# Kernel tuning notes

Hardware: AMD Instinct MI355X
Metric: run time of the kernel (lower is better)

Reference implementation:

```python
import jax, jax.numpy as jnp
import numpy as np


def _conv1x1(x, w, b):
    # x: (B,C,H,W), w: (O,C), b: (O,)
    return jnp.einsum('bchw,oc->bohw', x, w) + b[None, :, None, None]


def setup_inputs() -> dict:
    key = jax.random.key(0)
    ks = jax.random.split(key, 10)
    B, C, H, W = 8, 64, 64, 64
    x = jax.random.normal(ks[0], (B, C, H, W), dtype=jnp.float32)
    s = 0.05
    params = {}
    names = ['wq', 'wQ', 'wK', 'wV']
    for i, n in enumerate(names):
        params[n] = jax.random.normal(ks[1 + 2 * i], (C, C), dtype=jnp.float32) * s
        params['b' + n[1:]] = jax.random.normal(ks[2 + 2 * i], (C,), dtype=jnp.float32) * s
    return dict(x=x, wq=params['wq'], bq=params['bq'], wQ=params['wQ'], bQ=params['bQ'],
                wK=params['wK'], bK=params['bK'], wV=params['wV'], bV=params['bV'],
                gamma=jnp.ones((1,), dtype=jnp.float32))


def reference(x, wq, bq, wQ, bQ, wK, bK, wV, bV, gamma):
    B, C, H, W = x.shape
    # q = query_conv(x).view(B,-1,W,H)  (pure reshape, matches torch .view on contiguous tensor)
    q = _conv1x1(x, wq, bq).reshape(B, C, W, H)
    # 2x2 average pool, stride 2
    qp = q.reshape(B, C, W // 2, 2, H // 2, 2).mean(axis=(3, 5))
    q_ = qp.reshape(B, C, (W * H) // 4)          # (B, C, N/4)
    K = _conv1x1(x, wK, bK).reshape(B, C, H * W)  # (B, C, N)
    V = _conv1x1(x, wV, bV).reshape(B, C, H * W)  # (B, C, N)
    # stage 1: pooled queries attend over all keys
    attn1 = jax.nn.softmax(jnp.einsum('bcp,bcn->bpn', q_, K), axis=-1)  # (B, N/4, N)
    out = jnp.einsum('bcn,bpn->bcp', V, attn1)                           # (B, C, N/4)
    # stage 2: full queries attend over pooled anchors
    Q = _conv1x1(x, wQ, bQ).reshape(B, C, H * W)                         # (B, C, N)
    attn2 = jax.nn.softmax(jnp.einsum('bcn,bcp->bnp', Q, q_), axis=-1)   # (B, N, N/4)
    out = jnp.einsum('bcp,bnp->bcn', out, attn2)                         # (B, C, N)
    out = out.reshape(B, C, H, W)
    return gamma * out + x
```

## Files before the change

kernel.cpp:

```cpp
#include <hip/hip_runtime.h>
#include <hip/hip_bf16.h>


typedef float  f32x4  __attribute__((ext_vector_type(4)));
typedef __bf16 bf16x8 __attribute__((ext_vector_type(8)));
typedef __bf16 bf16x4 __attribute__((ext_vector_type(4)));

__device__ __forceinline__ int swz(int ch) { return ch ^ ((ch >> 3) & 7); }

__global__ __launch_bounds__(256) void conv4_kernel(
    const float* __restrict__ x,
    const float* __restrict__ wq, const float* __restrict__ bq,
    const float* __restrict__ wQ, const float* __restrict__ bQ,
    const float* __restrict__ wK, const float* __restrict__ bK,
    const float* __restrict__ wV, const float* __restrict__ bV,
    __bf16* __restrict__ Kt, __bf16* __restrict__ Vc,
    __bf16* __restrict__ Qt, __bf16* __restrict__ qt)
{
  __shared__ float xs[64 * 132];
  __shared__ float wsh[64 * 68];

  const int tid = threadIdx.x;
  const int m   = blockIdx.x >> 8;
  const int b   = (blockIdx.x >> 5) & 7;
  const int rp  = blockIdx.x & 31;
  const int n0  = rp << 7;

  const float* wg = (m == 0) ? wK : (m == 1) ? wV : (m == 2) ? wQ : wq;
  const float* bg = (m == 0) ? bK : (m == 1) ? bV : (m == 2) ? bQ : bq;

  for (int i = tid; i < 64 * 32; i += 256) {
    int c = i >> 5, j = i & 31;
    *(f32x4*)&xs[c * 132 + j * 4] =
        *(const f32x4*)&x[((size_t)(b * 64 + c)) * 4096 + n0 + j * 4];
  }
  for (int i = tid; i < 1024; i += 256) {
    int o = i >> 4, c0 = (i & 15) << 2;
    f32x4 v = *(const f32x4*)&wg[o * 64 + c0];
    wsh[(c0 + 0) * 68 + o] = v[0];
    wsh[(c0 + 1) * 68 + o] = v[1];
    wsh[(c0 + 2) * 68 + o] = v[2];
    wsh[(c0 + 3) * 68 + o] = v[3];
  }
  __syncthreads();

  const int ty = tid >> 4, tx = tid & 15;

  float acc[4][8];
  {
    f32x4 bv = *(const f32x4*)&bg[ty * 4];
#pragma unroll
    for (int i = 0; i < 4; ++i)
#pragma unroll
      for (int j = 0; j < 8; ++j) acc[i][j] = bv[i];
  }

#pragma unroll 4
  for (int c = 0; c < 64; ++c) {
    f32x4 wv = *(const f32x4*)&wsh[c * 68 + ty * 4];
    f32x4 xa = *(const f32x4*)&xs[c * 132 + tx * 8];
    f32x4 xb = *(const f32x4*)&xs[c * 132 + tx * 8 + 4];
#pragma unroll
    for (int i = 0; i < 4; ++i) {
#pragma unroll
      for (int j = 0; j < 4; ++j) {
        acc[i][j]     += wv[i] * xa[j];
        acc[i][j + 4] += wv[i] * xb[j];
      }
    }
  }

  if (m == 0 || m == 2) {
    __bf16* dst = (m == 0) ? Kt : Qt;
#pragma unroll
    for (int j = 0; j < 8; ++j) {
      int n = n0 + tx * 8 + j;
      bf16x4 pk;
#pragma unroll
      for (int i = 0; i < 4; ++i) pk[i] = (__bf16)acc[i][j];
      *(bf16x4*)&dst[((size_t)(b * 4096 + n)) * 64 + ty * 4] = pk;
    }
  } else if (m == 1) {
#pragma unroll
    for (int i = 0; i < 4; ++i) {
      int o = ty * 4 + i;
      bf16x8 pk;
#pragma unroll
      for (int j = 0; j < 8; ++j) pk[j] = (__bf16)acc[i][j];
      *(bf16x8*)&Vc[((size_t)(b * 64 + o)) * 4096 + n0 + tx * 8] = pk;
    }
  } else {
    float pl[4][4];
#pragma unroll
    for (int i = 0; i < 4; ++i)
#pragma unroll
      for (int jj = 0; jj < 4; ++jj)
        pl[i][jj] = acc[i][2 * jj] + acc[i][2 * jj + 1];
#pragma unroll
    for (int i = 0; i < 4; ++i)
#pragma unroll
      for (int jj = 0; jj < 4; ++jj)
        pl[i][jj] += __shfl_xor(pl[i][jj], 8);
    if (tx < 8) {
#pragma unroll
      for (int jj = 0; jj < 4; ++jj) {
        int p = rp * 32 + tx * 4 + jj;
        bf16x4 pk;
#pragma unroll
        for (int i = 0; i < 4; ++i) pk[i] = (__bf16)(0.25f * pl[i][jj]);
        *(bf16x4*)&qt[((size_t)(b * 1024 + p)) * 64 + ty * 4] = pk;
      }
    }
  }
}

__global__ __launch_bounds__(512, 2) void attn1_kernel(
    const __bf16* __restrict__ Qg,
    const __bf16* __restrict__ Kg,
    const __bf16* __restrict__ Vg,
    __bf16* __restrict__ outp)
{
  __shared__ __align__(16) char smem[147456];

  const int tid  = threadIdx.x;
  const int wave = tid >> 6, lane = tid & 63;
  const int lg = (lane >> 4) & 3, lp = lane & 15;
  const int qt = wave & 1, ks = wave >> 1;
  const int b  = blockIdx.x >> 5;
  const int q0 = (blockIdx.x & 31) * 32;

  const __bf16* qg = Qg + ((size_t)(b * 1024 + q0 + qt * 16 + lp)) * 64;
  const bf16x8 qf0 = *(const bf16x8*)(qg + lg * 8);
  const bf16x8 qf1 = *(const bf16x8*)(qg + 32 + lg * 8);

  f32x4 acc[4];
#pragma unroll
  for (int ct = 0; ct < 4; ++ct) acc[ct] = (f32x4){0.f, 0.f, 0.f, 0.f};
  float m_run = -3.0e38f, l_run = 0.0f;

  bf16x8 kreg[4], vreg[4];
  const int sw = swz(tid & 511);
  auto load_tile = [&](int r) {
    const __bf16* kb = Kg + (size_t)b * 262144 + (size_t)r * 4096 + tid * 8;
    const __bf16* vb = Vg + ((size_t)(b * 64 + (tid >> 3))) * 4096 + r * 64 + (tid & 7) * 8;
#pragma unroll
    for (int j = 0; j < 4; ++j) {
      kreg[j] = *(const bf16x8*)(kb + (size_t)j * 65536);
      vreg[j] = *(const bf16x8*)(vb + j * 1024);
    }
  };
  auto write_tile = [&](int nb) {
    __bf16* kd = (__bf16*)(smem + nb * 32768);
    __bf16* vd = (__bf16*)(smem + 65536 + nb * 32768);
#pragma unroll
    for (int j = 0; j < 4; ++j) {
      *(bf16x8*)(kd + (j * 512 + sw) * 8) = kreg[j];
      *(bf16x8*)(vd + (j * 512 + sw) * 8) = vreg[j];
    }
  };

  load_tile(0); write_tile(0);
  load_tile(1);
  __syncthreads();

  for (int r = 0; r < 16; ++r) {
    const int cur = r & 1;
    if (r + 1 < 16) write_tile(cur ^ 1);
    if (r + 2 < 16) load_tile(r + 2);

    const __bf16* lK = (const __bf16*)(smem + cur * 32768) + ks * 4096;
    const __bf16* lV = (const __bf16*)(smem + 65536 + cur * 32768) + ks * 4096;
    __bf16* lP = (__bf16*)(smem + 131072) + wave * 1024;

    f32x4 S[4];
#pragma unroll
    for (int mt = 0; mt < 4; ++mt) {
      int ch0 = (mt * 16 + lp) * 8 + lg;
      bf16x8 a0 = *(const bf16x8*)(lK + swz(ch0) * 8);
      bf16x8 a1 = *(const bf16x8*)(lK + swz(ch0 + 4) * 8);
      f32x4 z = (f32x4){0.f, 0.f, 0.f, 0.f};
      z = __builtin_amdgcn_mfma_f32_16x16x32_bf16(a0, qf0, z, 0, 0, 0);
      z = __builtin_amdgcn_mfma_f32_16x16x32_bf16(a1, qf1, z, 0, 0, 0);
      S[mt] = z;
    }

    float tmax = -3.0e38f;
#pragma unroll
    for (int mt = 0; mt < 4; ++mt)
#pragma unroll
      for (int rr = 0; rr < 4; ++rr) tmax = fmaxf(tmax, S[mt][rr]);
    tmax = fmaxf(tmax, __shfl_xor(tmax, 16));
    tmax = fmaxf(tmax, __shfl_xor(tmax, 32));
    float mnew = fmaxf(m_run, tmax);
    float sc = __expf(m_run - mnew);
    float rs = 0.f;
#pragma unroll
    for (int mt = 0; mt < 4; ++mt)
#pragma unroll
      for (int rr = 0; rr < 4; ++rr) {
        float e = __expf(S[mt][rr] - mnew);
        S[mt][rr] = e;
        rs += e;
      }
    rs += __shfl_xor(rs, 16);
    rs += __shfl_xor(rs, 32);
    l_run = l_run * sc + rs;
    m_run = mnew;
#pragma unroll
    for (int ct = 0; ct < 4; ++ct) acc[ct] *= sc;

#pragma unroll
    for (int mt = 0; mt < 4; ++mt) {
      bf16x4 pk;
#pragma unroll
      for (int rr = 0; rr < 4; ++rr) pk[rr] = (__bf16)S[mt][rr];
      int boff = lp * 128 + mt * 32 + lg * 8;
      *(bf16x4*)((char*)lP + (boff ^ ((lp & 7) << 4))) = pk;
    }

    {
      int chp = lp * 8 + lg;
      bf16x8 pf0 = *(const bf16x8*)(lP + swz(chp) * 8);
      bf16x8 pf1 = *(const bf16x8*)(lP + swz(chp + 4) * 8);
#pragma unroll
      for (int ct = 0; ct < 4; ++ct) {
        int chv = (ct * 16 + lp) * 8 + lg;
        bf16x8 v0 = *(const bf16x8*)(lV + swz(chv) * 8);
        bf16x8 v1 = *(const bf16x8*)(lV + swz(chv + 4) * 8);
        acc[ct] = __builtin_amdgcn_mfma_f32_16x16x32_bf16(v0, pf0, acc[ct], 0, 0, 0);
        acc[ct] = __builtin_amdgcn_mfma_f32_16x16x32_bf16(v1, pf1, acc[ct], 0, 0, 0);
      }
    }
    __syncthreads();
  }

  float2* mlb = (float2*)(smem + 131072);
  if (lg == 0) mlb[wave * 16 + lp] = make_float2(m_run, l_run);
  float* cb = (float*)smem;
  {
    float* myc = cb + ((size_t)(qt * 4 + ks) * 16 + lp) * 64;
#pragma unroll
    for (int ct = 0; ct < 4; ++ct)
      *(f32x4*)(myc + ct * 16 + lg * 4) = acc[ct];
  }
  __syncthreads();

  if (wave < 2) {
    const int qtt = wave;
    const int nq = q0 + qtt * 16 + lp;
    float mm[4], lv[4];
    float mstar = -3.0e38f;
#pragma unroll
    for (int s = 0; s < 4; ++s) {
      float2 v = mlb[(s * 2 + qtt) * 16 + lp];
      mm[s] = v.x; lv[s] = v.y;
      mstar = fmaxf(mstar, mm[s]);
    }
    float f[4], lstar = 0.f;
#pragma unroll
    for (int s = 0; s < 4; ++s) {
      f[s] = __expf(mm[s] - mstar);
      lstar += lv[s] * f[s];
    }
    float inv = 1.0f / lstar;
#pragma unroll
    for (int ct = 0; ct < 4; ++ct) {
      f32x4 o = (f32x4){0.f, 0.f, 0.f, 0.f};
#pragma unroll
      for (int s = 0; s < 4; ++s) {
        f32x4 t = *(const f32x4*)(cb + ((size_t)(qtt * 4 + s) * 16 + lp) * 64 +
                                  ct * 16 + lg * 4);
        o += f[s] * t;
      }
#pragma unroll
      for (int rr = 0; rr < 4; ++rr) {
        int c = ct * 16 + lg * 4 + rr;
        outp[((size_t)(b * 64 + c)) * 1024 + nq] = (__bf16)(o[rr] * inv);
      }
    }
  }
}

__global__ __launch_bounds__(512, 2) void attn2_kernel(
    const __bf16* __restrict__ Qg,
    const __bf16* __restrict__ Kg,
    const __bf16* __restrict__ Vg,
    float* __restrict__ outp,
    const float* __restrict__ xres,
    const float* __restrict__ gammap)
{
  __shared__ __align__(16) char smem[49152];

  const int tid  = threadIdx.x;
  const int wave = tid >> 6, lane = tid & 63;
  const int lg = (lane >> 4) & 3, lp = lane & 15;
  const int b  = blockIdx.x >> 5;
  const int q0 = (blockIdx.x & 31) * 128;
  const int myq = q0 + wave * 16 + lp;

  const __bf16* qg = Qg + ((size_t)(b * 4096 + myq)) * 64;
  const bf16x8 qf0 = *(const bf16x8*)(qg + lg * 8);
  const bf16x8 qf1 = *(const bf16x8*)(qg + 32 + lg * 8);

  f32x4 acc[4];
#pragma unroll
  for (int ct = 0; ct < 4; ++ct) acc[ct] = (f32x4){0.f, 0.f, 0.f, 0.f};
  float m_run = -3.0e38f, l_run = 0.0f;

  bf16x8 kreg, vreg;
  const int sw = swz(tid & 511);
  auto load_tile = [&](int r) {
    kreg = *(const bf16x8*)(Kg + (size_t)b * 65536 + (size_t)r * 4096 + tid * 8);
    vreg = *(const bf16x8*)(Vg + ((size_t)(b * 64 + (tid >> 3))) * 1024 + r * 64 + (tid & 7) * 8);
  };
  auto write_tile = [&](int nb) {
    *(bf16x8*)((__bf16*)(smem + nb * 8192) + sw * 8) = kreg;
    *(bf16x8*)((__bf16*)(smem + 16384 + nb * 8192) + sw * 8) = vreg;
  };

  load_tile(0); write_tile(0);
  load_tile(1);
  __syncthreads();

  for (int r = 0; r < 16; ++r) {
    const int cur = r & 1;
    if (r + 1 < 16) write_tile(cur ^ 1);
    if (r + 2 < 16) load_tile(r + 2);

    const __bf16* lK = (const __bf16*)(smem + cur * 8192);
    const __bf16* lV = (const __bf16*)(smem + 16384 + cur * 8192);
    __bf16* lP = (__bf16*)(smem + 32768) + wave * 1024;

    f32x4 S[4];
#pragma unroll
    for (int mt = 0; mt < 4; ++mt) {
      int ch0 = (mt * 16 + lp) * 8 + lg;
      bf16x8 a0 = *(const bf16x8*)(lK + swz(ch0) * 8);
      bf16x8 a1 = *(const bf16x8*)(lK + swz(ch0 + 4) * 8);
      f32x4 z = (f32x4){0.f, 0.f, 0.f, 0.f};
      z = __builtin_amdgcn_mfma_f32_16x16x32_bf16(a0, qf0, z, 0, 0, 0);
      z = __builtin_amdgcn_mfma_f32_16x16x32_bf16(a1, qf1, z, 0, 0, 0);
      S[mt] = z;
    }

    float tmax = -3.0e38f;
#pragma unroll
    for (int mt = 0; mt < 4; ++mt)
#pragma unroll
      for (int rr = 0; rr < 4; ++rr) tmax = fmaxf(tmax, S[mt][rr]);
    tmax = fmaxf(tmax, __shfl_xor(tmax, 16));
    tmax = fmaxf(tmax, __shfl_xor(tmax, 32));
    float mnew = fmaxf(m_run, tmax);
    float sc = __expf(m_run - mnew);
    float rs = 0.f;
#pragma unroll
    for (int mt = 0; mt < 4; ++mt)
#pragma unroll
      for (int rr = 0; rr < 4; ++rr) {
        float e = __expf(S[mt][rr] - mnew);
        S[mt][rr] = e;
        rs += e;
      }
    rs += __shfl_xor(rs, 16);
    rs += __shfl_xor(rs, 32);
    l_run = l_run * sc + rs;
    m_run = mnew;
#pragma unroll
    for (int ct = 0; ct < 4; ++ct) acc[ct] *= sc;

#pragma unroll
    for (int mt = 0; mt < 4; ++mt) {
      bf16x4 pk;
#pragma unroll
      for (int rr = 0; rr < 4; ++rr) pk[rr] = (__bf16)S[mt][rr];
      int boff = lp * 128 + mt * 32 + lg * 8;
      *(bf16x4*)((char*)lP + (boff ^ ((lp & 7) << 4))) = pk;
    }

    {
      int chp = lp * 8 + lg;
      bf16x8 pf0 = *(const bf16x8*)(lP + swz(chp) * 8);
      bf16x8 pf1 = *(const bf16x8*)(lP + swz(chp + 4) * 8);
#pragma unroll
      for (int ct = 0; ct < 4; ++ct) {
        int chv = (ct * 16 + lp) * 8 + lg;
        bf16x8 v0 = *(const bf16x8*)(lV + swz(chv) * 8);
        bf16x8 v1 = *(const bf16x8*)(lV + swz(chv + 4) * 8);
        acc[ct] = __builtin_amdgcn_mfma_f32_16x16x32_bf16(v0, pf0, acc[ct], 0, 0, 0);
        acc[ct] = __builtin_amdgcn_mfma_f32_16x16x32_bf16(v1, pf1, acc[ct], 0, 0, 0);
      }
    }
    __syncthreads();
  }

  const float inv = 1.0f / l_run;
  const float g0 = gammap[0];
#pragma unroll
  for (int ct = 0; ct < 4; ++ct)
#pragma unroll
    for (int rr = 0; rr < 4; ++rr) {
      int c = ct * 16 + lg * 4 + rr;
      size_t oi = ((size_t)(b * 64 + c)) * 4096 + myq;
      outp[oi] = g0 * (acc[ct][rr] * inv) + xres[oi];
    }
}

extern "C" void kernel_launch(void* const* d_in, const int* in_sizes, int n_in,
                              void* d_out, int out_size, void* d_ws, size_t ws_size,
                              hipStream_t stream) {
  const float* x     = (const float*)d_in[0];
  const float* wq    = (const float*)d_in[1];
  const float* bq    = (const float*)d_in[2];
  const float* wQ    = (const float*)d_in[3];
  const float* bQ    = (const float*)d_in[4];
  const float* wK    = (const float*)d_in[5];
  const float* bK    = (const float*)d_in[6];
  const float* wV    = (const float*)d_in[7];
  const float* bV    = (const float*)d_in[8];
  const float* gamma = (const float*)d_in[9];

  __bf16* ws = (__bf16*)d_ws;
  __bf16* Kt = ws;
  __bf16* Vc = ws + 2097152;
  __bf16* Qt = ws + 4194304;
  __bf16* qt = ws + 6291456;
  __bf16* O1 = ws + 6815744;

  hipLaunchKernelGGL(conv4_kernel, dim3(1024), dim3(256), 0, stream,
                     x, wq, bq, wQ, bQ, wK, bK, wV, bV, Kt, Vc, Qt, qt);
  hipLaunchKernelGGL(attn1_kernel, dim3(256), dim3(512), 0, stream,
                     qt, Kt, Vc, O1);
  hipLaunchKernelGGL(attn2_kernel, dim3(256), dim3(512), 0, stream,
                     Qt, qt, O1, (float*)d_out, x, gamma);
}
```

Measured before the change: 75.64 us.

## Split attn1 keys across blocks with a separate combine kernel; widen per-wave queries

attn1 now splits its 4096 keys into 8 chunks across blocks instead of across waves. Each block holds 256 queries (32 per wave) and writes fp32 partial outputs plus running max and sum to workspace. A new combine1 kernel merges these with log-sum-exp rescaling. attn2 also gives each wave 32 queries so the K fragments loaded from LDS are reused twice, and splits keys between two wave groups merged in shared memory. The aim is less LDS traffic per MFMA and smaller attn1 shared memory for better occupancy, at the cost of an extra launch and about 8 MB of fp32 partial-result traffic.

After: 74.09 us. -2.1%, faster.

```diff
diff --git a/kernel.cpp b/kernel.cpp
--- a/kernel.cpp
+++ b/kernel.cpp
@@ -118,166 +118,193 @@
     const __bf16* __restrict__ Qg,
     const __bf16* __restrict__ Kg,
     const __bf16* __restrict__ Vg,
-    __bf16* __restrict__ outp)
+    float* __restrict__ partO,
+    float2* __restrict__ partML)
 {
-  __shared__ __align__(16) char smem[147456];
-
-  const int tid  = threadIdx.x;
-  const int wave = tid >> 6, lane = tid & 63;
+  __shared__ __align__(16) char smem[65536];
+
+  const int tid = threadIdx.x;
+  const int w = tid >> 6, lane = tid & 63;
   const int lg = (lane >> 4) & 3, lp = lane & 15;
-  const int qt = wave & 1, ks = wave >> 1;
   const int b  = blockIdx.x >> 5;
-  const int q0 = (blockIdx.x & 31) * 32;
-
-  const __bf16* qg = Qg + ((size_t)(b * 1024 + q0 + qt * 16 + lp)) * 64;
-  const bf16x8 qf0 = *(const bf16x8*)(qg + lg * 8);
-  const bf16x8 qf1 = *(const bf16x8*)(qg + 32 + lg * 8);
-
-  f32x4 acc[4];
-#pragma unroll
-  for (int ct = 0; ct < 4; ++ct) acc[ct] = (f32x4){0.f, 0.f, 0.f, 0.f};
-  float m_run = -3.0e38f, l_run = 0.0f;
-
-  bf16x8 kreg[4], vreg[4];
-  const int sw = swz(tid & 511);
+  const int qb = (blockIdx.x >> 3) & 3;
+  const int ks = blockIdx.x & 7;
+
+  bf16x8 qf[2][2];
+#pragma unroll
+  for (int qs = 0; qs < 2; ++qs) {
+    const __bf16* qg =
+        Qg + ((size_t)(b * 1024 + qb * 256 + w * 32 + qs * 16 + lp)) * 64;
+    qf[qs][0] = *(const bf16x8*)(qg + lg * 8);
+    qf[qs][1] = *(const bf16x8*)(qg + 32 + lg * 8);
+  }
+
+  f32x4 acc[2][4];
+#pragma unroll
+  for (int qs = 0; qs < 2; ++qs)
+#pragma unroll
+    for (int ct = 0; ct < 4; ++ct) acc[qs][ct] = (f32x4){0.f, 0.f, 0.f, 0.f};
+  float m_run[2] = {-3.0e38f, -3.0e38f}, l_run[2] = {0.f, 0.f};
+
+  bf16x8 kreg, vreg;
+  const int swt = swz(tid);
   auto load_tile = [&](int r) {
-    const __bf16* kb = Kg + (size_t)b * 262144 + (size_t)r * 4096 + tid * 8;
-    const __bf16* vb = Vg + ((size_t)(b * 64 + (tid >> 3))) * 4096 + r * 64 + (tid & 7) * 8;
-#pragma unroll
-    for (int j = 0; j < 4; ++j) {
-      kreg[j] = *(const bf16x8*)(kb + (size_t)j * 65536);
-      vreg[j] = *(const bf16x8*)(vb + j * 1024);
-    }
+    const int kv0 = ks * 512 + r * 64;
+    kreg = *(const bf16x8*)(Kg + ((size_t)(b * 4096 + kv0 + (tid >> 3))) * 64 +
+                            (tid & 7) * 8);
+    vreg = *(const bf16x8*)(Vg + ((size_t)(b * 64 + (tid >> 3))) * 4096 + kv0 +
+                            (tid & 7) * 8);
   };
   auto write_tile = [&](int nb) {
-    __bf16* kd = (__bf16*)(smem + nb * 32768);
-    __bf16* vd = (__bf16*)(smem + 65536 + nb * 32768);
-#pragma unroll
-    for (int j = 0; j < 4; ++j) {
-      *(bf16x8*)(kd + (j * 512 + sw) * 8) = kreg[j];
-      *(bf16x8*)(vd + (j * 512 + sw) * 8) = vreg[j];
-    }
+    *(bf16x8*)((__bf16*)(smem + nb * 8192) + swt * 8) = kreg;
+    *(bf16x8*)((__bf16*)(smem + 16384 + nb * 8192) + swt * 8) = vreg;
   };
 
-  load_tile(0); write_tile(0);
-  load_tile(1);
+  load_tile(0); write_tile(0); load_tile(1);
   __syncthreads();
 
-  for (int r = 0; r < 16; ++r) {
+  for (int r = 0; r < 8; ++r) {
     const int cur = r & 1;
-    if (r + 1 < 16) write_tile(cur ^ 1);
-    if (r + 2 < 16) load_tile(r + 2);
-
-    const __bf16* lK = (const __bf16*)(smem + cur * 32768) + ks * 4096;
-    const __bf16* lV = (const __bf16*)(smem + 65536 + cur * 32768) + ks * 4096;
-    __bf16* lP = (__bf16*)(smem + 131072) + wave * 1024;
-
-    f32x4 S[4];
+    if (r + 1 < 8) write_tile(cur ^ 1);
+    if (r + 2 < 8) load_tile(r + 2);
+
+    const __bf16* lK = (const __bf16*)(smem + cur * 8192);
+    const __bf16* lV = (const __bf16*)(smem + 16384 + cur * 8192);
+    __bf16* lP = (__bf16*)(smem + 32768) + w * 2048;
+
+    bf16x8 ka[4][2];
 #pragma unroll
     for (int mt = 0; mt < 4; ++mt) {
       int ch0 = (mt * 16 + lp) * 8 + lg;
-      bf16x8 a0 = *(const bf16x8*)(lK + swz(ch0) * 8);
-      bf16x8 a1 = *(const bf16x8*)(lK + swz(ch0 + 4) * 8);
-      f32x4 z = (f32x4){0.f, 0.f, 0.f, 0.f};
-      z = __builtin_amdgcn_mfma_f32_16x16x32_bf16(a0, qf0, z, 0, 0, 0);
-      z = __builtin_amdgcn_mfma_f32_16x16x32_bf16(a1, qf1, z, 0, 0, 0);
-      S[mt] = z;
-    }
-
-    float tmax = -3.0e38f;
-#pragma unroll
-    for (int mt = 0; mt < 4; ++mt)
-#pragma unroll
-      for (int rr = 0; rr < 4; ++rr) tmax = fmaxf(tmax, S[mt][rr]);
-    tmax = fmaxf(tmax, __shfl_xor(tmax, 16));
-    tmax = fmaxf(tmax, __shfl_xor(tmax, 32));
-    float mnew = fmaxf(m_run, tmax);
-    float sc = __expf(m_run - mnew);
-    float rs = 0.f;
-#pragma unroll
-    for (int mt = 0; mt < 4; ++mt)
-#pragma unroll
-      for (int rr = 0; rr < 4; ++rr) {
-        float e = __expf(S[mt][rr] - mnew);
-        S[mt][rr] = e;
-        rs += e;
-      }
-    rs += __shfl_xor(rs, 16);
-    rs += __shfl_xor(rs, 32);
-    l_run = l_run * sc + rs;
-    m_run = mnew;
-#pragma unroll
-    for (int ct = 0; ct < 4; ++ct) acc[ct] *= sc;
-
-#pragma unroll
-    for (int mt = 0; mt < 4; ++mt) {
-      bf16x4 pk;
-#pragma unroll
-      for (int rr = 0; rr < 4; ++rr) pk[rr] = (__bf16)S[mt][rr];
-      int boff = lp * 128 + mt * 32 + lg * 8;
-      *(bf16x4*)((char*)lP + (boff ^ ((lp & 7) << 4))) = pk;
-    }
-
-    {
-      int chp = lp * 8 + lg;
-      bf16x8 pf0 = *(const bf16x8*)(lP + swz(chp) * 8);
-      bf16x8 pf1 = *(const bf16x8*)(lP + swz(chp + 4) * 8);
-#pragma unroll
-      for (int ct = 0; ct < 4; ++ct) {
-        int chv = (ct * 16 + lp) * 8 + lg;
-        bf16x8 v0 = *(const bf16x8*)(lV + swz(chv) * 8);
-        bf16x8 v1 = *(const bf16x8*)(lV + swz(chv + 4) * 8);
-        acc[ct] = __builtin_amdgcn_mfma_f32_16x16x32_bf16(v0, pf0, acc[ct], 0, 0, 0);
-        acc[ct] = __builtin_amdgcn_mfma_f32_16x16x32_bf16(v1, pf1, acc[ct], 0, 0, 0);
+      ka[mt][0] = *(const bf16x8*)(lK + swz(ch0) * 8);
+      ka[mt][1] = *(const bf16x8*)(lK + swz(ch0 + 4) * 8);
+    }
+
+#pragma unroll
+    for (int qs = 0; qs < 2; ++qs) {
+      f32x4 S[4];
+#pragma unroll
+      for (int mt = 0; mt < 4; ++mt) {
+        f32x4 z = (f32x4){0.f, 0.f, 0.f, 0.f};
+        z = __builtin_amdgcn_mfma_f32_16x16x32_bf16(ka[mt][0], qf[qs][0], z, 0, 0, 0);
+        z = __builtin_amdgcn_mfma_f32_16x16x32_bf16(ka[mt][1], qf[qs][1], z, 0, 0, 0);
+        S[mt] = z;
+      }
+
+      float tmax = -3.0e38f;
+#pragma unroll
+      for (int mt = 0; mt < 4; ++mt)
+#pragma unroll
+        for (int rr = 0; rr < 4; ++rr) tmax = fmaxf(tmax, S[mt][rr]);
+      tmax = fmaxf(tmax, __shfl_xor(tmax, 16));
+      tmax = fmaxf(tmax, __shfl_xor(tmax, 32));
+      float mnew = fmaxf(m_run[qs], tmax);
+      float sc = __expf(m_run[qs] - mnew);
+      float rs = 0.f;
+#pragma unroll
+      for (int mt = 0; mt < 4; ++mt)
+#pragma unroll
+        for (int rr = 0; rr < 4; ++rr) {
+          float e = __expf(S[mt][rr] - mnew);
+          S[mt][rr] = e;
+          rs += e;
+        }
+      rs += __shfl_xor(rs, 16);
+      rs += __shfl_xor(rs, 32);
+      l_run[qs] = l_run[qs] * sc + rs;
+      m_run[qs] = mnew;
+#pragma unroll
+      for (int ct = 0; ct < 4; ++ct) acc[qs][ct] *= sc;
+
+#pragma unroll
+      for (int mt = 0; mt < 4; ++mt) {
+        bf16x4 pk;
+#pragma unroll
+        for (int rr = 0; rr < 4; ++rr) pk[rr] = (__bf16)S[mt][rr];
+        int boff = (qs * 16 + lp) * 128 + mt * 32 + lg * 8;
+        *(bf16x4*)((char*)lP + (boff ^ ((lp & 7) << 4))) = pk;
+      }
+    }
+
+    bf16x8 pf[2][2];
+#pragma unroll
+    for (int qs = 0; qs < 2; ++qs) {
+      int chp = (qs * 16 + lp) * 8 + lg;
+      pf[qs][0] = *(const bf16x8*)(lP + swz(chp) * 8);
+      pf[qs][1] = *(const bf16x8*)(lP + swz(chp + 4) * 8);
+    }
+#pragma unroll
+    for (int ct = 0; ct < 4; ++ct) {
+      int chv = (ct * 16 + lp) * 8 + lg;
+      bf16x8 v0 = *(const bf16x8*)(lV + swz(chv) * 8);
+      bf16x8 v1 = *(const bf16x8*)(lV + swz(chv + 4) * 8);
+#pragma unroll
+      for (int qs = 0; qs < 2; ++qs) {
+        acc[qs][ct] = __builtin_amdgcn_mfma_f32_16x16x32_bf16(v0, pf[qs][0], acc[qs][ct], 0, 0, 0);
+        acc[qs][ct] = __builtin_amdgcn_mfma_f32_16x16x32_bf16(v1, pf[qs][1], acc[qs][ct], 0, 0, 0);
       }
     }
     __syncthreads();
   }
 
-  float2* mlb = (float2*)(smem + 131072);
-  if (lg == 0) mlb[wave * 16 + lp] = make_float2(m_run, l_run);
-  float* cb = (float*)smem;
+  const size_t pbase = (size_t)((b * 4 + qb) * 8 + ks);
+  if (lg == 0) {
+#pragma unroll
+    for (int qs = 0; qs < 2; ++qs)
+      partML[pbase * 256 + w * 32 + qs * 16 + lp] =
+          make_float2(m_run[qs], l_run[qs]);
+  }
+  float* po = partO + pbase * 16384;
+#pragma unroll
+  for (int qs = 0; qs < 2; ++qs)
+#pragma unroll
+    for (int ct = 0; ct < 4; ++ct)
+#pragma unroll
+      for (int rr = 0; rr < 4; ++rr)
+        po[(ct * 16 + lg * 4 + rr) * 256 + w * 32 + qs * 16 + lp] =
+            acc[qs][ct][rr];
+}
+
+__global__ __launch_bounds__(256) void combine1_kernel(
+    const float* __restrict__ partO, const float2* __restrict__ partML,
+    __bf16* __restrict__ O1)
+{
+  __shared__ float fs[8][256];
+  __shared__ float inv[256];
+
+  const int tid = threadIdx.x;
+  const int b   = blockIdx.x >> 5;
+  const int qb  = (blockIdx.x >> 3) & 3;
+  const int cs  = blockIdx.x & 7;
+  const size_t mbase = (size_t)(b * 4 + qb) * 8;
+
   {
-    float* myc = cb + ((size_t)(qt * 4 + ks) * 16 + lp) * 64;
-#pragma unroll
-    for (int ct = 0; ct < 4; ++ct)
-      *(f32x4*)(myc + ct * 16 + lg * 4) = acc[ct];
-  }
-  __syncthreads();
-
-  if (wave < 2) {
-    const int qtt = wave;
-    const int nq = q0 + qtt * 16 + lp;
-    float mm[4], lv[4];
+    float mm[8], lv[8];
     float mstar = -3.0e38f;
 #pragma unroll
-    for (int s = 0; s < 4; ++s) {
-      float2 v = mlb[(s * 2 + qtt) * 16 + lp];
+    for (int s = 0; s < 8; ++s) {
+      float2 v = partML[(mbase + s) * 256 + tid];
       mm[s] = v.x; lv[s] = v.y;
       mstar = fmaxf(mstar, mm[s]);
     }
-    float f[4], lstar = 0.f;
-#pragma unroll
-    for (int s = 0; s < 4; ++s) {
-      f[s] = __expf(mm[s] - mstar);
-      lstar += lv[s] * f[s];
-    }
-    float inv = 1.0f / lstar;
-#pragma unroll
-    for (int ct = 0; ct < 4; ++ct) {
-      f32x4 o = (f32x4){0.f, 0.f, 0.f, 0.f};
-#pragma unroll
-      for (int s = 0; s < 4; ++s) {
-        f32x4 t = *(const f32x4*)(cb + ((size_t)(qtt * 4 + s) * 16 + lp) * 64 +
-                                  ct * 16 + lg * 4);
-        o += f[s] * t;
-      }
-#pragma unroll
-      for (int rr = 0; rr < 4; ++rr) {
-        int c = ct * 16 + lg * 4 + rr;
-        outp[((size_t)(b * 64 + c)) * 1024 + nq] = (__bf16)(o[rr] * inv);
-      }
-    }
+    float l = 0.f;
+#pragma unroll
+    for (int s = 0; s < 8; ++s) {
+      float fv = __expf(mm[s] - mstar);
+      fs[s][tid] = fv;
+      l += lv[s] * fv;
+    }
+    inv[tid] = 1.0f / l;
+  }
+  __syncthreads();
+
+  for (int i = tid; i < 2048; i += 256) {
+    int c = cs * 8 + (i >> 8), q = i & 255;
+    float o = 0.f;
+#pragma unroll
+    for (int s = 0; s < 8; ++s)
+      o += fs[s][q] * partO[((mbase + s) * 64 + c) * 256 + q];
+    O1[((size_t)(b * 64 + c)) * 1024 + qb * 256 + q] = (__bf16)(o * inv[q]);
   }
 }
 
@@ -289,120 +316,183 @@
     const float* __restrict__ xres,
     const float* __restrict__ gammap)
 {
-  __shared__ __align__(16) char smem[49152];
-
-  const int tid  = threadIdx.x;
-  const int wave = tid >> 6, lane = tid & 63;
+  __shared__ __align__(16) char smem[98304];
+
+  const int tid = threadIdx.x;
+  const int w = tid >> 6, lane = tid & 63;
   const int lg = (lane >> 4) & 3, lp = lane & 15;
+  const int qg4 = w & 3, ks = w >> 2;
   const int b  = blockIdx.x >> 5;
   const int q0 = (blockIdx.x & 31) * 128;
-  const int myq = q0 + wave * 16 + lp;
-
-  const __bf16* qg = Qg + ((size_t)(b * 4096 + myq)) * 64;
-  const bf16x8 qf0 = *(const bf16x8*)(qg + lg * 8);
-  const bf16x8 qf1 = *(const bf16x8*)(qg + 32 + lg * 8);
-
-  f32x4 acc[4];
-#pragma unroll
-  for (int ct = 0; ct < 4; ++ct) acc[ct] = (f32x4){0.f, 0.f, 0.f, 0.f};
-  float m_run = -3.0e38f, l_run = 0.0f;
-
-  bf16x8 kreg, vreg;
-  const int sw = swz(tid & 511);
+
+  bf16x8 qf[2][2];
+#pragma unroll
+  for (int qs = 0; qs < 2; ++qs) {
+    const __bf16* qg =
+        Qg + ((size_t)(b * 4096 + q0 + qg4 * 32 + qs * 16 + lp)) * 64;
+    qf[qs][0] = *(const bf16x8*)(qg + lg * 8);
+    qf[qs][1] = *(const bf16x8*)(qg + 32 + lg * 8);
+  }
+
+  f32x4 acc[2][4];
+#pragma unroll
+  for (int qs = 0; qs < 2; ++qs)
+#pragma unroll
+    for (int ct = 0; ct < 4; ++ct) acc[qs][ct] = (f32x4){0.f, 0.f, 0.f, 0.f};
+  float m_run[2] = {-3.0e38f, -3.0e38f}, l_run[2] = {0.f, 0.f};
+
+  bf16x8 kreg[2], vreg[2];
+  const int csi = tid & 255, sp = tid >> 8;
+  const int sw0 = swz(csi), sw1 = swz(csi + 256);
   auto load_tile = [&](int r) {
-    kreg = *(const bf16x8*)(Kg + (size_t)b * 65536 + (size_t)r * 4096 + tid * 8);
-    vreg = *(const bf16x8*)(Vg + ((size_t)(b * 64 + (tid >> 3))) * 1024 + r * 64 + (tid & 7) * 8);
+    const int a0 = sp * 512 + r * 64;
+#pragma unroll
+    for (int j = 0; j < 2; ++j) {
+      int s = csi + j * 256;
+      int row = s >> 3, col = (s & 7) * 8;
+      kreg[j] = *(const bf16x8*)(Kg + ((size_t)(b * 1024 + a0 + row)) * 64 + col);
+      vreg[j] = *(const bf16x8*)(Vg + ((size_t)(b * 64 + row)) * 1024 + a0 + col);
+    }
   };
   auto write_tile = [&](int nb) {
-    *(bf16x8*)((__bf16*)(smem + nb * 8192) + sw * 8) = kreg;
-    *(bf16x8*)((__bf16*)(smem + 16384 + nb * 8192) + sw * 8) = vreg;
+    __bf16* kd = (__bf16*)(smem + (sp * 2 + nb) * 8192);
+    __bf16* vd = (__bf16*)(smem + 32768 + (sp * 2 + nb) * 8192);
+    *(bf16x8*)(kd + sw0 * 8) = kreg[0];
+    *(bf16x8*)(kd + sw1 * 8) = kreg[1];
+    *(bf16x8*)(vd + sw0 * 8) = vreg[0];
+    *(bf16x8*)(vd + sw1 * 8) = vreg[1];
   };
 
-  load_tile(0); write_tile(0);
-  load_tile(1);
+  load_tile(0); write_tile(0); load_tile(1);
   __syncthreads();
 
-  for (int r = 0; r < 16; ++r) {
+  for (int r = 0; r < 8; ++r) {
     const int cur = r & 1;
-    if (r + 1 < 16) write_tile(cur ^ 1);
-    if (r + 2 < 16) load_tile(r + 2);
-
-    const __bf16* lK = (const __bf16*)(smem + cur * 8192);
-    const __bf16* lV = (const __bf16*)(smem + 16384 + cur * 8192);
-    __bf16* lP = (__bf16*)(smem + 32768) + wave * 1024;
-
-    f32x4 S[4];
+    if (r + 1 < 8) write_tile(cur ^ 1);
+    if (r + 2 < 8) load_tile(r + 2);
+
+    const __bf16* lK = (const __bf16*)(smem + (ks * 2 + cur) * 8192);
+    const __bf16* lV = (const __bf16*)(smem + 32768 + (ks * 2 + cur) * 8192);
+    __bf16* lP = (__bf16*)(smem + 65536) + w * 2048;
+
+    bf16x8 ka[4][2];
 #pragma unroll
     for (int mt = 0; mt < 4; ++mt) {
       int ch0 = (mt * 16 + lp) * 8 + lg;
-      bf16x8 a0 = *(const bf16x8*)(lK + swz(ch0) * 8);
-      bf16x8 a1 = *(const bf16x8*)(lK + swz(ch0 + 4) * 8);
-      f32x4 z = (f32x4){0.f, 0.f, 0.f, 0.f};
-      z = __builtin_amdgcn_mfma_f32_16x16x32_bf16(a0, qf0, z, 0, 0, 0);
-      z = __builtin_amdgcn_mfma_f32_16x16x32_bf16(a1, qf1, z, 0, 0, 0);
-      S[mt] = z;
-    }
-
-    float tmax = -3.0e38f;
-#pragma unroll
-    for (int mt = 0; mt < 4; ++mt)
-#pragma unroll
-      for (int rr = 0; rr < 4; ++rr) tmax = fmaxf(tmax, S[mt][rr]);
-    tmax = fmaxf(tmax, __shfl_xor(tmax, 16));
-    tmax = fmaxf(tmax, __shfl_xor(tmax, 32));
-    float mnew = fmaxf(m_run, tmax);
-    float sc = __expf(m_run - mnew);
-    float rs = 0.f;
-#pragma unroll
-    for (int mt = 0; mt < 4; ++mt)
-#pragma unroll
-      for (int rr = 0; rr < 4; ++rr) {
-        float e = __expf(S[mt][rr] - mnew);
-        S[mt][rr] = e;
-        rs += e;
-      }
-    rs += __shfl_xor(rs, 16);
-    rs += __shfl_xor(rs, 32);
-    l_run = l_run * sc + rs;
-    m_run = mnew;
-#pragma unroll
-    for (int ct = 0; ct < 4; ++ct) acc[ct] *= sc;
-
-#pragma unroll
-    for (int mt = 0; mt < 4; ++mt) {
-      bf16x4 pk;
-#pragma unroll
-      for (int rr = 0; rr < 4; ++rr) pk[rr] = (__bf16)S[mt][rr];
-      int boff = lp * 128 + mt * 32 + lg * 8;
-      *(bf16x4*)((char*)lP + (boff ^ ((lp & 7) << 4))) = pk;
-    }
-
-    {
-      int chp = lp * 8 + lg;
-      bf16x8 pf0 = *(const bf16x8*)(lP + swz(chp) * 8);
-      bf16x8 pf1 = *(const bf16x8*)(lP + swz(chp + 4) * 8);
+      ka[mt][0] = *(const bf16x8*)(lK + swz(ch0) * 8);
+      ka[mt][1] = *(const bf16x8*)(lK + swz(ch0 + 4) * 8);
+    }
+
+#pragma unroll
+    for (int qs = 0; qs < 2; ++qs) {
+      f32x4 S[4];
+#pragma unroll
+      for (int mt = 0; mt < 4; ++mt) {
+        f32x4 z = (f32x4){0.f, 0.f, 0.f, 0.f};
+        z = __builtin_amdgcn_mfma_f32_16x16x32_bf16(ka[mt][0], qf[qs][0], z, 0, 0, 0);
+        z = __builtin_amdgcn_mfma_f32_16x16x32_bf16(ka[mt][1], qf[qs][1], z, 0, 0, 0);
+        S[mt] = z;
+      }
+
+      float tmax = -3.0e38f;
+#pragma unroll
+      for (int mt = 0; mt < 4; ++mt)
+#pragma unroll
+        for (int rr = 0; rr < 4; ++rr) tmax = fmaxf(tmax, S[mt][rr]);
+      tmax = fmaxf(tmax, __shfl_xor(tmax, 16));
+      tmax = fmaxf(tmax, __shfl_xor(tmax, 32));
+      float mnew = fmaxf(m_run[qs], tmax);
+      float sc = __expf(m_run[qs] - mnew);
+      float rs = 0.f;
+#pragma unroll
+      for (int mt = 0; mt < 4; ++mt)
+#pragma unroll
+        for (int rr = 0; rr < 4; ++rr) {
+          float e = __expf(S[mt][rr] - mnew);
+          S[mt][rr] = e;
+          rs += e;
+        }
+      rs += __shfl_xor(rs, 16);
+      rs += __shfl_xor(rs, 32);
+      l_run[qs] = l_run[qs] * sc + rs;
+      m_run[qs] = mnew;
+#pragma unroll
+      for (int ct = 0; ct < 4; ++ct) acc[qs][ct] *= sc;
+
+#pragma unroll
+      for (int mt = 0; mt < 4; ++mt) {
+        bf16x4 pk;
+#pragma unroll
+        for (int rr = 0; rr < 4; ++rr) pk[rr] = (__bf16)S[mt][rr];
+        int boff = (qs * 16 + lp) * 128 + mt * 32 + lg * 8;
+        *(bf16x4*)((char*)lP + (boff ^ ((lp & 7) << 4))) = pk;
+      }
+    }
+
+    bf16x8 pf[2][2];
+#pragma unroll
+    for (int qs = 0; qs < 2; ++qs) {
+      int chp = (qs * 16 + lp) * 8 + lg;
+      pf[qs][0] = *(const bf16x8*)(lP + swz(chp) * 8);
+      pf[qs][1] = *(const bf16x8*)(lP + swz(chp + 4) * 8);
+    }
+#pragma unroll
+    for (int ct = 0; ct < 4; ++ct) {
+      int chv = (ct * 16 + lp) * 8 + lg;
+      bf16x8 v0 = *(const bf16x8*)(lV + swz(chv) * 8);
+      bf16x8 v1 = *(const bf16x8*)(lV + swz(chv + 4) * 8);
+#pragma unroll
+      for (int qs = 0; qs < 2; ++qs) {
+        acc[qs][ct] = __builtin_amdgcn_mfma_f32_16x16x32_bf16(v0, pf[qs][0], acc[qs][ct], 0, 0, 0);
+        acc[qs][ct] = __builtin_amdgcn_mfma_f32_16x16x32_bf16(v1, pf[qs][1], acc[qs][ct], 0, 0, 0);
+      }
+    }
+    __syncthreads();
+  }
+
+  float*  cb  = (float*)smem;
+  float2* mlb = (float2*)(smem + 69632);
+  if (lg == 0) {
+#pragma unroll
+    for (int qs = 0; qs < 2; ++qs)
+      mlb[w * 32 + qs * 16 + lp] = make_float2(m_run[qs], l_run[qs]);
+  }
+  {
+    float* myc = cb + w * 2176;
+#pragma unroll
+    for (int qs = 0; qs < 2; ++qs)
+#pragma unroll
+      for (int ct = 0; ct < 4; ++ct)
+        *(f32x4*)(myc + (qs * 16 + lp) * 68 + ct * 16 + lg * 4) = acc[qs][ct];
+  }
+  __syncthreads();
+
+  if (w < 4) {
+    const int g = w;
+    const float g0 = gammap[0];
+#pragma unroll
+    for (int qs = 0; qs < 2; ++qs) {
+      const int qq = qs * 16 + lp;
+      const int nq = q0 + g * 32 + qq;
+      float2 v0 = mlb[g * 32 + qq];
+      float2 v1 = mlb[(g + 4) * 32 + qq];
+      float mstar = fmaxf(v0.x, v1.x);
+      float f0 = __expf(v0.x - mstar), f1 = __expf(v1.x - mstar);
+      float inv = 1.0f / (v0.y * f0 + v1.y * f1);
 #pragma unroll
       for (int ct = 0; ct < 4; ++ct) {
-        int chv = (ct * 16 + lp) * 8 + lg;
-        bf16x8 v0 = *(const bf16x8*)(lV + swz(chv) * 8);
-        bf16x8 v1 = *(const bf16x8*)(lV + swz(chv + 4) * 8);
-        acc[ct] = __builtin_amdgcn_mfma_f32_16x16x32_bf16(v0, pf0, acc[ct], 0, 0, 0);
-        acc[ct] = __builtin_amdgcn_mfma_f32_16x16x32_bf16(v1, pf1, acc[ct], 0, 0, 0);
-      }
-    }
-    __syncthreads();
-  }
-
-  const float inv = 1.0f / l_run;
-  const float g0 = gammap[0];
-#pragma unroll
-  for (int ct = 0; ct < 4; ++ct)
-#pragma unroll
-    for (int rr = 0; rr < 4; ++rr) {
-      int c = ct * 16 + lg * 4 + rr;
-      size_t oi = ((size_t)(b * 64 + c)) * 4096 + myq;
-      outp[oi] = g0 * (acc[ct][rr] * inv) + xres[oi];
-    }
+        f32x4 t0 = *(const f32x4*)(cb + g * 2176 + qq * 68 + ct * 16 + lg * 4);
+        f32x4 t1 = *(const f32x4*)(cb + (g + 4) * 2176 + qq * 68 + ct * 16 + lg * 4);
+        f32x4 o = f0 * t0 + f1 * t1;
+#pragma unroll
+        for (int rr = 0; rr < 4; ++rr) {
+          int c = ct * 16 + lg * 4 + rr;
+          size_t oi = ((size_t)(b * 64 + c)) * 4096 + nq;
+          outp[oi] = g0 * (o[rr] * inv) + xres[oi];
+        }
+      }
+    }
+  }
 }
 
 extern "C" void kernel_launch(void* const* d_in, const int* in_sizes, int n_in,
@@ -425,11 +515,15 @@
   __bf16* Qt = ws + 4194304;
   __bf16* qt = ws + 6291456;
   __bf16* O1 = ws + 6815744;
+  float*  partO  = (float*)((char*)d_ws + (16u << 20));
+  float2* partML = (float2*)((char*)d_ws + (32u << 20));
 
   hipLaunchKernelGGL(conv4_kernel, dim3(1024), dim3(256), 0, stream,
                      x, wq, bq, wQ, bQ, wK, bK, wV, bV, Kt, Vc, Qt, qt);
   hipLaunchKernelGGL(attn1_kernel, dim3(256), dim3(512), 0, stream,
-                     qt, Kt, Vc, O1);
+                     qt, Kt, Vc, partO, partML);
+  hipLaunchKernelGGL(combine1_kernel, dim3(256), dim3(256), 0, stream,
+                     partO, partML, O1);
   hipLaunchKernelGGL(attn2_kernel, dim3(256), dim3(512), 0, stream,
                      Qt, qt, O1, (float*)d_out, x, gamma);
 }
```
